# Optimization experiments

Hardware: AMD Instinct MI355X
Metric: run time of the kernel (lower is better)

## Reference

```python
import jax, jax.numpy as jnp
import numpy as np

S, I, H, C, B = 512, 1, 256, 10, 2048

def _xavier(key, shape):
    fan_out, fan_in = shape
    std = (2.0 / (fan_in + fan_out)) ** 0.5
    return jax.random.normal(key, shape, dtype=jnp.float32) * std

def setup_inputs() -> dict:
    key = jax.random.key(0)
    k_x, k_hx, k_hh, k_ph = jax.random.split(key, 4)
    return {
        "x": jax.random.normal(k_x, (B, S), dtype=jnp.float32),
        "W_hx": _xavier(k_hx, (H, I)),
        "W_hh": _xavier(k_hh, (H, H)),
        "W_ph": _xavier(k_ph, (C, H)),
        "b_h": jnp.zeros((H, 1), dtype=jnp.float32),
        "b_p": jnp.zeros((C, 1), dtype=jnp.float32),
    }

def reference(x, W_hx, W_hh, W_ph, b_h, b_p):
    # x: [B, S]; hidden state h: [H, B]
    batch = x.shape[0]
    h0 = jnp.zeros((W_hh.shape[0], batch), dtype=x.dtype)
    xs = x.T  # [S, B], one row per timestep

    def step(h, x_t):
        # x_t: [B] -> [1, B]; W_hx: [H, 1]
        h_new = jnp.tanh(W_hx @ x_t[None, :] + W_hh @ h + b_h)
        return h_new, None

    h_final, _ = jax.lax.scan(step, h0, xs)
    # output: [B, C]
    return (W_ph @ h_final + b_p).T
```

## Files before the change

kernel.cpp:

```cpp
#include <hip/hip_runtime.h>


#define SEQ    512
#define HID    256
#define NCLS   10
#define BN     8
#define NT     512
#define XPITCH 9

typedef _Float16 f16x8 __attribute__((ext_vector_type(8)));
typedef _Float16 f16x4 __attribute__((ext_vector_type(4)));
typedef float    f32x4 __attribute__((ext_vector_type(4)));

__global__ __launch_bounds__(NT)
__attribute__((amdgpu_waves_per_eu(2, 2)))
void rnn_mfma(
    const float* __restrict__ x,
    const float* __restrict__ W_hx,
    const float* __restrict__ W_hh,
    const float* __restrict__ W_ph,
    const float* __restrict__ b_h,
    const float* __restrict__ b_p,
    float* __restrict__ out)
{
    __shared__ __align__(16) _Float16 hT[2][BN][HID];
    __shared__ __align__(16) float xs[SEQ + 2][XPITCH];

    const int tid  = threadIdx.x;
    const int lane = tid & 63;
    const int wave = tid >> 6;
    const int n16  = lane & 15;
    const int quad = lane >> 4;
    const int nb   = n16 & 7;
    const int b0   = blockIdx.x * BN;

    const float SC = 2.885390081777926814f;

    f16x8 afrag[2][8];
#pragma unroll
    for (int mt = 0; mt < 2; ++mt) {
        const int row = wave * 32 + mt * 16 + n16;
#pragma unroll
        for (int ks = 0; ks < 8; ++ks) {
            const float4* p = (const float4*)&W_hh[row * HID + ks * 32 + quad * 8];
            float4 u = p[0], v = p[1];
            f16x8 a;
            a[0] = (_Float16)(SC * u.x); a[1] = (_Float16)(SC * u.y);
            a[2] = (_Float16)(SC * u.z); a[3] = (_Float16)(SC * u.w);
            a[4] = (_Float16)(SC * v.x); a[5] = (_Float16)(SC * v.y);
            a[6] = (_Float16)(SC * v.z); a[7] = (_Float16)(SC * v.w);
            afrag[mt][ks] = a;
        }
    }
    f32x4 bias[2], wxv[2];
#pragma unroll
    for (int mt = 0; mt < 2; ++mt)
#pragma unroll
        for (int r = 0; r < 4; ++r) {
            const int row = wave * 32 + mt * 16 + quad * 4 + r;
            bias[mt][r] = SC * b_h[row];
            wxv[mt][r]  = SC * W_hx[row];
        }

    int roff[8], woff[2];
#pragma unroll
    for (int ks = 0; ks < 8; ++ks)
        roff[ks] = (nb * HID + (((4 * ks + quad) ^ nb) << 3)) * 2;
#pragma unroll
    for (int mt = 0; mt < 2; ++mt)
        woff[mt] = (nb * HID +
                    (((4 * wave + 2 * mt + (quad >> 1)) ^ nb) << 3) +
                    (quad & 1) * 4) * 2;

    for (int i = tid; i < BN * SEQ / 4; i += NT) {
        const int n = i >> 7, t4 = (i & 127) * 4;
        float4 v = *(const float4*)&x[(b0 + n) * SEQ + t4];
        xs[t4 + 0][n] = v.x; xs[t4 + 1][n] = v.y;
        xs[t4 + 2][n] = v.z; xs[t4 + 3][n] = v.w;
    }
    for (int i = tid; i < BN * HID / 2; i += NT) ((float*)hT[0])[i] = 0.0f;
    __syncthreads();

    float xv = xs[0][nb];

#define RNN_STEP(T, RD, WR)                                                   \
    {                                                                         \
        const float xnxt = xs[(T) + 1][nb];       \
        const char* hb = (const char*)hT[RD];                                 \
        f16x8 bfr[8];                                                         \
        _Pragma("unroll")                                                     \
        for (int ks = 0; ks < 8; ++ks)                                        \
            bfr[ks] = *(const f16x8*)(hb + roff[ks]);                         \
        f32x4 acc0[2], acc1[2];                                               \
        _Pragma("unroll")                                                     \
        for (int mt = 0; mt < 2; ++mt) {                                      \
            f32x4 c0;                                                         \
            _Pragma("unroll")                                                 \
            for (int r = 0; r < 4; ++r)                                       \
                c0[r] = fmaf(wxv[mt][r], xv, bias[mt][r]);                    \
            acc0[mt] = __builtin_amdgcn_mfma_f32_16x16x32_f16(                \
                afrag[mt][0], bfr[0], c0, 0, 0, 0);                           \
            acc1[mt] = __builtin_amdgcn_mfma_f32_16x16x32_f16(                \
                afrag[mt][1], bfr[1], (f32x4)0.0f, 0, 0, 0);                  \
        }                                                                     \
        _Pragma("unroll")                                                     \
        for (int ks = 2; ks < 8; ks += 2)                                     \
            _Pragma("unroll")                                                 \
            for (int mt = 0; mt < 2; ++mt) {                                  \
                acc0[mt] = __builtin_amdgcn_mfma_f32_16x16x32_f16(            \
                    afrag[mt][ks], bfr[ks], acc0[mt], 0, 0, 0);               \
                acc1[mt] = __builtin_amdgcn_mfma_f32_16x16x32_f16(            \
                    afrag[mt][ks + 1], bfr[ks + 1], acc1[mt], 0, 0, 0);       \
            }                                                                 \
        char* wb = (char*)hT[WR];                                             \
        f16x4 h4[2];                                                          \
        _Pragma("unroll")                                                     \
        for (int mt = 0; mt < 2; ++mt)                                        \
            _Pragma("unroll")                                                 \
            for (int r = 0; r < 4; ++r) {                                     \
                float s  = acc0[mt][r] + acc1[mt][r];                         \
                float ex = __builtin_amdgcn_exp2f(s);                         \
                float rc = __builtin_amdgcn_rcpf(ex + 1.0f);                  \
                h4[mt][r] = (_Float16)(1.0f - 2.0f * rc);                     \
            }                                                                 \
        if (n16 < 8) {                                                        \
            *(f16x4*)(wb + woff[0]) = h4[0];                                  \
            *(f16x4*)(wb + woff[1]) = h4[1];                                  \
        }                                                                     \
        xv = xnxt;                                                            \
        __syncthreads();                                                      \
    }

    for (int t = 0; t < SEQ; t += 2) {
        RNN_STEP(t, 0, 1);
        RNN_STEP(t + 1, 1, 0);
    }
#undef RNN_STEP

    if (tid < BN * NCLS) {
        const int b = tid / NCLS, c = tid % NCLS;
        float sum = b_p[c];
        const _Float16* hp = hT[0][b];
        for (int j = 0; j < HID; ++j) {
            const int ph = ((((j >> 3) ^ b) << 3) | (j & 7));
            sum += W_ph[c * HID + j] * (float)hp[ph];
        }
        out[(b0 + b) * NCLS + c] = sum;
    }
}

extern "C" void kernel_launch(void* const* d_in, const int* in_sizes, int n_in,
                              void* d_out, int out_size, void* d_ws, size_t ws_size,
                              hipStream_t stream) {
    const float* x    = (const float*)d_in[0];
    const float* W_hx = (const float*)d_in[1];
    const float* W_hh = (const float*)d_in[2];
    const float* W_ph = (const float*)d_in[3];
    const float* b_h  = (const float*)d_in[4];
    const float* b_p  = (const float*)d_in[5];
    float* out = (float*)d_out;

    rnn_mfma<<<dim3(2048 / BN), dim3(NT), 0, stream>>>(
        x, W_hx, W_hh, W_ph, b_h, b_p, out);
}
```

Before: 340.7 us.

## Process 16 batch columns per block to fill MFMA N dimension

Doubles the batch tile per block from 8 to 16 so all 16 N-columns of each 16x16x32 MFMA carry real batch elements instead of duplicating 8. This halves the grid to 128 blocks and the number of sequential recurrence chains. The LDS swizzle for h is changed to a 16-row pattern to avoid bank conflicts, and every lane now writes h. The x-projection term moves into the second accumulator's initial value. With 128 blocks on a 256-CU device, half the CUs sit idle, but each block does the same per-step latency work, so total time should roughly halve.

```diff
diff --git a/kernel.cpp b/kernel.cpp
--- a/kernel.cpp
+++ b/kernel.cpp
@@ -4,9 +4,9 @@
 #define SEQ    512
 #define HID    256
 #define NCLS   10
-#define BN     8
+#define BN     16
 #define NT     512
-#define XPITCH 9
+#define XP     17
 
 typedef _Float16 f16x8 __attribute__((ext_vector_type(8)));
 typedef _Float16 f16x4 __attribute__((ext_vector_type(4)));
@@ -24,14 +24,14 @@
     float* __restrict__ out)
 {
     __shared__ __align__(16) _Float16 hT[2][BN][HID];
-    __shared__ __align__(16) float xs[SEQ + 2][XPITCH];
+    __shared__ __align__(16) float xs[SEQ + 2][XP];
 
     const int tid  = threadIdx.x;
     const int lane = tid & 63;
     const int wave = tid >> 6;
     const int n16  = lane & 15;
     const int quad = lane >> 4;
-    const int nb   = n16 & 7;
+    const int sw   = (n16 & 7) ^ ((n16 >> 3) << 2);
     const int b0   = blockIdx.x * BN;
 
     const float SC = 2.885390081777926814f;
@@ -65,11 +65,11 @@
     int roff[8], woff[2];
 #pragma unroll
     for (int ks = 0; ks < 8; ++ks)
-        roff[ks] = (nb * HID + (((4 * ks + quad) ^ nb) << 3)) * 2;
+        roff[ks] = (n16 * HID + (((4 * ks + quad) ^ sw) << 3)) * 2;
 #pragma unroll
     for (int mt = 0; mt < 2; ++mt)
-        woff[mt] = (nb * HID +
-                    (((4 * wave + 2 * mt + (quad >> 1)) ^ nb) << 3) +
+        woff[mt] = (n16 * HID +
+                    (((4 * wave + 2 * mt + (quad >> 1)) ^ sw) << 3) +
                     (quad & 1) * 4) * 2;
 
     for (int i = tid; i < BN * SEQ / 4; i += NT) {
@@ -81,11 +81,11 @@
     for (int i = tid; i < BN * HID / 2; i += NT) ((float*)hT[0])[i] = 0.0f;
     __syncthreads();
 
-    float xv = xs[0][nb];
+    float xv = xs[0][n16];
 
 #define RNN_STEP(T, RD, WR)                                                   \
     {                                                                         \
-        const float xnxt = xs[(T) + 1][nb];       \
+        const float xnxt = xs[(T) + 1][n16];      \
         const char* hb = (const char*)hT[RD];                                 \
         f16x8 bfr[8];                                                         \
         _Pragma("unroll")                                                     \
@@ -94,14 +94,16 @@
         f32x4 acc0[2], acc1[2];                                               \
         _Pragma("unroll")                                                     \
         for (int mt = 0; mt < 2; ++mt) {                                      \
-            f32x4 c0;                                                         \
+            f32x4 c0, c1;                                                     \
             _Pragma("unroll")                                                 \
-            for (int r = 0; r < 4; ++r)                                       \
-                c0[r] = fmaf(wxv[mt][r], xv, bias[mt][r]);                    \
+            for (int r = 0; r < 4; ++r) {                                     \
+                c0[r] = bias[mt][r];                                          \
+                c1[r] = wxv[mt][r] * xv;                                      \
+            }                                                                 \
             acc0[mt] = __builtin_amdgcn_mfma_f32_16x16x32_f16(                \
                 afrag[mt][0], bfr[0], c0, 0, 0, 0);                           \
             acc1[mt] = __builtin_amdgcn_mfma_f32_16x16x32_f16(                \
-                afrag[mt][1], bfr[1], (f32x4)0.0f, 0, 0, 0);                  \
+                afrag[mt][1], bfr[1], c1, 0, 0, 0);                           \
         }                                                                     \
         _Pragma("unroll")                                                     \
         for (int ks = 2; ks < 8; ks += 2)                                     \
@@ -113,19 +115,17 @@
                     afrag[mt][ks + 1], bfr[ks + 1], acc1[mt], 0, 0, 0);       \
             }                                                                 \
         char* wb = (char*)hT[WR];                                             \
-        f16x4 h4[2];                                                          \
         _Pragma("unroll")                                                     \
-        for (int mt = 0; mt < 2; ++mt)                                        \
+        for (int mt = 0; mt < 2; ++mt) {                                      \
+            f16x4 h4;                                                         \
             _Pragma("unroll")                                                 \
             for (int r = 0; r < 4; ++r) {                                     \
                 float s  = acc0[mt][r] + acc1[mt][r];                         \
                 float ex = __builtin_amdgcn_exp2f(s);                         \
                 float rc = __builtin_amdgcn_rcpf(ex + 1.0f);                  \
-                h4[mt][r] = (_Float16)(1.0f - 2.0f * rc);                     \
+                h4[r] = (_Float16)(1.0f - 2.0f * rc);                         \
             }                                                                 \
-        if (n16 < 8) {                                                        \
-            *(f16x4*)(wb + woff[0]) = h4[0];                                  \
-            *(f16x4*)(wb + woff[1]) = h4[1];                                  \
+            *(f16x4*)(wb + woff[mt]) = h4;                                    \
         }                                                                     \
         xv = xnxt;                                                            \
         __syncthreads();                                                      \
@@ -139,10 +139,11 @@
 
     if (tid < BN * NCLS) {
         const int b = tid / NCLS, c = tid % NCLS;
+        const int sb = (b & 7) ^ ((b >> 3) << 2);
         float sum = b_p[c];
         const _Float16* hp = hT[0][b];
         for (int j = 0; j < HID; ++j) {
-            const int ph = ((((j >> 3) ^ b) << 3) | (j & 7));
+            const int ph = ((((j >> 3) ^ sb) << 3) | (j & 7));
             sum += W_ph[c * HID + j] * (float)hp[ph];
         }
         out[(b0 + b) * NCLS + c] = sum;
```

After: 353.7 us. +3.8%, slower.
